# Kernel tuning notes

Measured on AMD Instinct MI355X. Metric: run time of the kernel, lower is better.

## Reference

```python
import jax, jax.numpy as jnp
import numpy as np

N, E, T, D, A = 16384, 65536, 2048, 64, 6


def _w(k, shape, fan_in):
    return jax.random.normal(k, shape, jnp.float32) / np.sqrt(fan_in)


def setup_inputs() -> dict:
    key = jax.random.key(0)
    ks = jax.random.split(key, 20)
    inp = {}
    inp["x"] = jax.random.normal(ks[0], (N, 3), jnp.float32)
    inp["edge_attr"] = jax.random.normal(ks[1], (E, 7), jnp.float32)
    inp["edge_index"] = jax.random.randint(ks[2], (2, E), 0, N)
    inp["nonring"] = jax.random.randint(ks[3], (T, 4), 0, N)
    inp["hx"] = jnp.zeros((1, D), jnp.float32)
    inp["cx"] = jnp.zeros((1, D), jnp.float32)
    inp["W_lin0"] = _w(ks[4], (D, 3), 3); inp["b_lin0"] = jnp.zeros((D,), jnp.float32)
    inp["W_e1"] = _w(ks[5], (128, 7), 7); inp["b_e1"] = jnp.zeros((128,), jnp.float32)
    inp["W_e2"] = _w(ks[6], (D * D, 128), 128); inp["b_e2"] = jnp.zeros((D * D,), jnp.float32)
    inp["conv_root"] = _w(ks[7], (D, D), D); inp["conv_bias"] = jnp.zeros((D,), jnp.float32)
    inp["gru_Wih"] = _w(ks[8], (3 * D, D), D); inp["gru_Whh"] = _w(ks[9], (3 * D, D), D)
    inp["gru_bih"] = jnp.zeros((3 * D,), jnp.float32); inp["gru_bhh"] = jnp.zeros((3 * D,), jnp.float32)
    inp["s2s_Wih"] = _w(ks[10], (4 * D, 2 * D), 2 * D); inp["s2s_Whh"] = _w(ks[11], (4 * D, D), D)
    inp["s2s_bih"] = jnp.zeros((4 * D,), jnp.float32); inp["s2s_bhh"] = jnp.zeros((4 * D,), jnp.float32)
    inp["mem_Wih"] = _w(ks[12], (4 * D, 2 * D), 2 * D); inp["mem_Whh"] = _w(ks[13], (4 * D, D), D)
    inp["mem_bih"] = jnp.zeros((4 * D,), jnp.float32); inp["mem_bhh"] = jnp.zeros((4 * D,), jnp.float32)
    inp["W_lin1"] = _w(ks[14], (D, 5 * D), 5 * D); inp["b_lin1"] = jnp.zeros((D,), jnp.float32)
    inp["W_lin2"] = _w(ks[15], (A, D), D); inp["b_lin2"] = jnp.zeros((A,), jnp.float32)
    inp["W_lin3"] = _w(ks[16], (1, 3 * D), 3 * D); inp["b_lin3"] = jnp.zeros((1,), jnp.float32)
    return inp


def _lstm_cell(xin, h, c, Wih, Whh, bih, bhh):
    g = xin @ Wih.T + bih + h @ Whh.T + bhh
    i, f, gg, o = jnp.split(g, 4, axis=-1)  # torch gate order i,f,g,o
    c = jax.nn.sigmoid(f) * c + jax.nn.sigmoid(i) * jnp.tanh(gg)
    h = jax.nn.sigmoid(o) * jnp.tanh(c)
    return h, c


def _gru_cell(xin, h, Wih, Whh, bih, bhh):
    gi = xin @ Wih.T + bih
    gh = h @ Whh.T + bhh
    ir, iz, inn = jnp.split(gi, 3, axis=-1)  # torch gate order r,z,n
    hr, hz, hn = jnp.split(gh, 3, axis=-1)
    r = jax.nn.sigmoid(ir + hr)
    z = jax.nn.sigmoid(iz + hz)
    n = jnp.tanh(inn + r * hn)
    return (1.0 - z) * n + z * h


def reference(x, edge_attr, edge_index, nonring, hx, cx,
              W_lin0, b_lin0, W_e1, b_e1, W_e2, b_e2, conv_root, conv_bias,
              gru_Wih, gru_Whh, gru_bih, gru_bhh,
              s2s_Wih, s2s_Whh, s2s_bih, s2s_bhh,
              mem_Wih, mem_Whh, mem_bih, mem_bhh,
              W_lin1, b_lin1, W_lin2, b_lin2, W_lin3, b_lin3):
    src, tgt = edge_index[0], edge_index[1]
    out = jax.nn.relu(x @ W_lin0.T + b_lin0)  # [N, D]
    h = out  # GRU hidden (nodes as batch)
    # edge-conditioned dim x dim matrices (NNConv edge MLP)
    ew = jax.nn.relu(edge_attr @ W_e1.T + b_e1)
    ew = (ew @ W_e2.T + b_e2).reshape(E, D, D)  # [E, D, D]
    cnt = jnp.maximum(jax.ops.segment_sum(jnp.ones((E,), out.dtype), tgt, num_segments=N), 1.0)
    for _ in range(3):
        msg = jnp.einsum('ed,edf->ef', out[src], ew)  # per-edge small matmul
        aggr = jax.ops.segment_sum(msg, tgt, num_segments=N) / cnt[:, None]  # scatter-mean
        m = jax.nn.relu(aggr + out @ conv_root + conv_bias)  # NNConv root + bias, then relu
        h = _gru_cell(m, h, gru_Wih, gru_Whh, gru_bih, gru_bhh)
        out = h
    # Set2Set pooling (single graph, B=1), processing_steps=3
    hs = jnp.zeros((1, D), out.dtype)
    cs = jnp.zeros((1, D), out.dtype)
    q_star = jnp.zeros((1, 2 * D), out.dtype)
    for _ in range(3):
        hs, cs = _lstm_cell(q_star, hs, cs, s2s_Wih, s2s_Whh, s2s_bih, s2s_bhh)
        a = jax.nn.softmax(out @ hs[0])  # [N]
        r = (a[:, None] * out).sum(0, keepdims=True)  # [1, D]
        q_star = jnp.concatenate([hs, r], axis=1)
    pool = q_star  # [1, 2D]
    lstm_out, cx_new = _lstm_cell(pool, hx, cx, mem_Wih, mem_Whh, mem_bih, mem_bhh)
    hx_new = lstm_out
    # torsion head: index_select -> view(4*D, -1) -> permute(1,0)
    sel = out[nonring.reshape(-1)]  # [4T, D]
    tfeat = sel.reshape(4 * D, -1).T  # [T, 4D], faithful to torch view semantics
    rep = jnp.repeat(lstm_out.reshape(-1), T).reshape(T, D)  # torch repeat_interleave + view
    pf = jnp.concatenate([tfeat, rep], axis=1)  # [T, 5D]
    logits = jax.nn.relu(pf @ W_lin1.T + b_lin1) @ W_lin2.T + b_lin2  # [T, A]
    v = jnp.concatenate([pool, lstm_out], axis=1) @ W_lin3.T + b_lin3  # [1, 1]
    return logits, v, hx_new, cx_new
```

## Files before the change

### kernel.cpp

```cpp
#include <hip/hip_runtime.h>

#define cN 16384
#define cE 65536
#define cT 2048
#define CAP 88

typedef __attribute__((ext_vector_type(8))) short short8;
typedef __attribute__((ext_vector_type(4))) float f32x4;
typedef __attribute__((ext_vector_type(4))) unsigned u32x4;

__device__ __forceinline__ short f2bf(float f){
  unsigned u = __float_as_uint(f);
  u = (u + 0x7FFFu + ((u >> 16) & 1u)) >> 16;
  return (short)u;
}
__device__ __forceinline__ float bf2f(short s){
  return __uint_as_float(((unsigned)(unsigned short)s) << 16);
}
__device__ __forceinline__ unsigned cvtpk(float lo, float hi){
  unsigned r;
  asm("v_cvt_pk_bf16_f32 %0, %1, %2" : "=v"(r) : "v"(lo), "v"(hi));
  return r;
}
__device__ __forceinline__ float sigm(float x){ return 1.f / (1.f + __expf(-x)); }
__device__ __forceinline__ float wred(float v){
  v += __shfl_xor(v, 32); v += __shfl_xor(v, 16); v += __shfl_xor(v, 8);
  v += __shfl_xor(v, 4);  v += __shfl_xor(v, 2);  v += __shfl_xor(v, 1);
  return v;
}
__device__ __forceinline__ float wredmax(float v){
  v = fmaxf(v, __shfl_xor(v, 32)); v = fmaxf(v, __shfl_xor(v, 16));
  v = fmaxf(v, __shfl_xor(v, 8));  v = fmaxf(v, __shfl_xor(v, 4));
  v = fmaxf(v, __shfl_xor(v, 2));  v = fmaxf(v, __shfl_xor(v, 1));
  return v;
}

#define B_L0   4096
#define B_H1   20480
#define B_W2   22528
#define B_B2   22544
#define B_WP   22656
#define B_DEG  22912
__global__ __launch_bounds__(256) void k_setup(
    const float* __restrict__ x, const float* __restrict__ Wl0, const float* __restrict__ bl0,
    float* __restrict__ out,
    const float* __restrict__ ea, const float* __restrict__ We1, const float* __restrict__ be1,
    unsigned* __restrict__ h1p,
    const float* __restrict__ W2, short* __restrict__ w2f,
    const float* __restrict__ b2, short* __restrict__ b2f,
    const float* __restrict__ convW, const float* __restrict__ gWih,
    const float* __restrict__ gWhh, short* __restrict__ wpk,
    const int* __restrict__ ei, int* __restrict__ deg)
{
  int b = blockIdx.x, tid = threadIdx.x;
  if (b < B_L0){
    int i = b * 256 + tid;
    int n = i >> 6, f = i & 63;
    float acc = bl0[f] + x[n*3]*Wl0[f*3] + x[n*3+1]*Wl0[f*3+1] + x[n*3+2]*Wl0[f*3+2];
    out[i] = fmaxf(acc, 0.f);
  } else if (b < B_H1){
    int i = (b - B_L0) * 256 + tid;
    int e = i >> 6, k = i & 63;
    const float* a  = ea + e * 7;
    const float* w0 = We1 + k * 7;
    const float* w1 = We1 + (k + 64) * 7;
    float a0 = be1[k], a1 = be1[k + 64];
    #pragma unroll
    for (int c = 0; c < 7; c++){ float av = a[c]; a0 += av * w0[c]; a1 += av * w1[c]; }
    unsigned lo = (unsigned short)f2bf(fmaxf(a0, 0.f));
    unsigned hi = (unsigned short)f2bf(fmaxf(a1, 0.f));
    h1p[i] = lo | (hi << 16);
  } else if (b < B_W2){
    int o = (b - B_H1) * 256 + tid;
    int j = o & 7, l = (o >> 3) & 63, ks = (o >> 9) & 31, c = (o >> 14) & 7, fb = (o >> 17) & 3;
    int f = fb * 16 + (l & 15);
    int d = c * 8 + j;
    int k = ks * 4 + ((l >> 4) & 3);
    w2f[o] = f2bf(W2[(d * 64 + f) * 128 + k]);
  } else if (b < B_B2){
    int o = (b - B_W2) * 256 + tid;
    int j = o & 7, l = (o >> 3) & 63, ks2 = (o >> 9) & 1, fb = (o >> 10) & 3;
    int d = ks2 * 32 + ((l >> 4) & 3) * 8 + j;
    int f = fb * 16 + (l & 15);
    b2f[o] = f2bf(b2[d * 64 + f]);
  } else if (b < B_WP){
    int o = (b - B_B2) * 256 + tid;
    int j = o & 7, l = (o >> 3) & 63, kc = (o >> 9) & 1, cb = o >> 10;
    int k = kc * 32 + ((l >> 4) & 3) * 8 + j;
    int c16 = l & 15;
    float v;
    if (cb < 4)       v = convW[k * 64 + cb * 16 + c16];
    else if (cb < 16) v = gWih[((cb - 4) * 16 + c16) * 64 + k];
    else              v = gWhh[((cb - 16) * 16 + c16) * 64 + k];
    wpk[o] = f2bf(v);
  } else {
    int e = (b - B_WP) * 256 + tid;
    atomicAdd(&deg[ei[cE + e]], 1);
  }
}

__global__ __launch_bounds__(1024) void k_scan(const int* __restrict__ deg,
    int* __restrict__ rowp, float* __restrict__ cnt)
{
  __shared__ int part[1024];
  int tid = threadIdx.x;
  int base = tid * 16;
  int loc[16]; int s = 0;
  #pragma unroll
  for (int i = 0; i < 16; i++){ loc[i] = s; s += deg[base + i]; }
  part[tid] = s;
  __syncthreads();
  for (int off = 1; off < 1024; off <<= 1){
    int v = (tid >= off) ? part[tid - off] : 0;
    __syncthreads();
    part[tid] += v;
    __syncthreads();
  }
  int inc = part[tid];
  int eb = inc - s;
  #pragma unroll
  for (int i = 0; i < 16; i++){
    rowp[base + i] = eb + loc[i];
    int dv = deg[base + i];
    cnt[base + i] = (float)(dv > 0 ? dv : 1);
  }
  if (tid == 1023) rowp[16384] = inc;
}

__global__ __launch_bounds__(256) void k_scatter(const int* __restrict__ ei,
    const int* __restrict__ rowp, int* __restrict__ cur,
    int* __restrict__ esrc, int* __restrict__ eidx)
{
  int e = blockIdx.x * 256 + threadIdx.x;
  int t = ei[cE + e];
  int pos = rowp[t] + atomicAdd(&cur[t], 1);
  esrc[pos] = ei[e];
  eidx[pos] = e;
}

__global__ __launch_bounds__(256) void k_sagg(const float* __restrict__ outR,
    float* __restrict__ outW,
    const unsigned* __restrict__ h1p, const short* __restrict__ w2f,
    const short* __restrict__ b2f, const short* __restrict__ wpk,
    const float* __restrict__ convB, const float* __restrict__ bih,
    const float* __restrict__ bhh, const float* __restrict__ cnt,
    const int* __restrict__ rowp, const int* __restrict__ esrc,
    const int* __restrict__ eidx)
{
  __shared__ __align__(16) short S[16][1040];
  __shared__ __align__(16) unsigned h1i[CAP][64];
  __shared__ __align__(16) float outsf[CAP][64];
  __shared__ __align__(16) short osb[16][72];
  int tid = threadIdx.x, w = tid >> 6, lane = tid & 63;
  int t0 = blockIdx.x * 16;

  int ebase = rowp[t0];
  int eend  = rowp[t0 + 16];
  int ecnt  = eend - ebase;
  bool fits = (ecnt <= CAP);
  int scnt  = fits ? ecnt : CAP;
  for (int i = w; i < scnt; i += 4){
    int eid = eidx[ebase + i];
    int src = esrc[ebase + i];
    h1i[i][lane] = h1p[(size_t)eid * 64 + lane];
    outsf[i][lane] = outR[(size_t)src * 64 + lane];
  }
  int toff[4], tcnt[4];
  #pragma unroll
  for (int g = 0; g < 4; g++){
    int t = t0 + w * 4 + g;
    int a = rowp[t], b = rowp[t + 1];
    toff[g] = a - ebase; tcnt[g] = b - a;
  }
  __syncthreads();

  #pragma unroll
  for (int g = 0; g < 4; g++){
    int ti = w * 4 + g;
    float os = 0.f;
    int tf = toff[g], tc = tcnt[g];
    for (int p = 0; p < tc; p++){
      int slot = tf + p;
      if (slot < CAP) os += outsf[slot][lane];
      else            os += outR[(size_t)esrc[ebase + slot] * 64 + lane];
    }
    osb[ti][lane] = (short)cvtpk(os, os);
  }

  f32x4 acc[4] = {{0,0,0,0},{0,0,0,0},{0,0,0,0},{0,0,0,0}};
  int arow = lane & 15, kg = lane >> 4;
  for (int c = 0; c < 8; ++c){
    #pragma unroll
    for (int g = 0; g < 4; ++g){
      int ti = w * 4 + g;
      float a0[8], a1[8];
      #pragma unroll
      for (int d = 0; d < 8; d++){ a0[d] = 0.f; a1[d] = 0.f; }
      int tc = tcnt[g], tf = toff[g];
      if (fits){
        #pragma unroll 2
        for (int p = 0; p < tc; ++p){
          int slot = tf + p;
          unsigned u = h1i[slot][lane];
          float h1a = __uint_as_float(u << 16);
          float h1b = __uint_as_float(u & 0xFFFF0000u);
          f32x4 o0 = *(const f32x4*)&outsf[slot][c * 8];
          f32x4 o1 = *(const f32x4*)&outsf[slot][c * 8 + 4];
          a0[0] = fmaf(o0[0], h1a, a0[0]); a1[0] = fmaf(o0[0], h1b, a1[0]);
          a0[1] = fmaf(o0[1], h1a, a0[1]); a1[1] = fmaf(o0[1], h1b, a1[1]);
          a0[2] = fmaf(o0[2], h1a, a0[2]); a1[2] = fmaf(o0[2], h1b, a1[2]);
          a0[3] = fmaf(o0[3], h1a, a0[3]); a1[3] = fmaf(o0[3], h1b, a1[3]);
          a0[4] = fmaf(o1[0], h1a, a0[4]); a1[4] = fmaf(o1[0], h1b, a1[4]);
          a0[5] = fmaf(o1[1], h1a, a0[5]); a1[5] = fmaf(o1[1], h1b, a1[5]);
          a0[6] = fmaf(o1[2], h1a, a0[6]); a1[6] = fmaf(o1[2], h1b, a1[6]);
          a0[7] = fmaf(o1[3], h1a, a0[7]); a1[7] = fmaf(o1[3], h1b, a1[7]);
        }
      } else {
        for (int p = 0; p < tc; ++p){
          int slot = tf + p;
          if (slot < CAP){
            unsigned u = h1i[slot][lane];
            float h1a = __uint_as_float(u << 16);
            float h1b = __uint_as_float(u & 0xFFFF0000u);
            f32x4 o0 = *(const f32x4*)&outsf[slot][c * 8];
            f32x4 o1 = *(const f32x4*)&outsf[slot][c * 8 + 4];
            #pragma unroll
            for (int d = 0; d < 4; d++){
              a0[d] = fmaf(o0[d], h1a, a0[d]); a1[d] = fmaf(o0[d], h1b, a1[d]);
              a0[4+d] = fmaf(o1[d], h1a, a0[4+d]); a1[4+d] = fmaf(o1[d], h1b, a1[4+d]);
            }
          } else {
            int eid = eidx[ebase + slot];
            int src = esrc[ebase + slot];
            unsigned u = h1p[(size_t)eid * 64 + lane];
            float h1a = __uint_as_float(u << 16);
            float h1b = __uint_as_float(u & 0xFFFF0000u);
            #pragma unroll
            for (int d = 0; d < 8; d++){
              float o = outR[(size_t)src * 64 + c * 8 + d];
              a0[d] = fmaf(o, h1a, a0[d]); a1[d] = fmaf(o, h1b, a1[d]);
            }
          }
        }
      }
      u32x4 p0, p1;
      p0[0] = cvtpk(a0[0], a0[1]); p0[1] = cvtpk(a0[2], a0[3]);
      p0[2] = cvtpk(a0[4], a0[5]); p0[3] = cvtpk(a0[6], a0[7]);
      p1[0] = cvtpk(a1[0], a1[1]); p1[1] = cvtpk(a1[2], a1[3]);
      p1[2] = cvtpk(a1[4], a1[5]); p1[3] = cvtpk(a1[6], a1[7]);
      *(u32x4*)&S[ti][lane * 8]       = p0;
      *(u32x4*)&S[ti][512 + lane * 8] = p1;
    }
    __syncthreads();
    const short* bbase = w2f + ((size_t)(w * 8 + c) * 32) * 512 + lane * 8;
    #pragma unroll
    for (int ks8 = 0; ks8 < 8; ++ks8){
      #pragma unroll
      for (int j = 0; j < 4; ++j){
        int ks = ks8 * 4 + j;
        short8 afr = *(const short8*)&S[arow][ks * 32 + kg * 8];
        short8 bfr = *(const short8*)(bbase + (size_t)ks * 512);
        acc[j] = __builtin_amdgcn_mfma_f32_16x16x32_bf16(afr, bfr, acc[j], 0, 0, 0);
      }
    }
    __syncthreads();
  }
  #pragma unroll
  for (int ks2 = 0; ks2 < 2; ++ks2){
    short8 osf = *(const short8*)&osb[arow][ks2 * 32 + kg * 8];
    short8 bfr = *(const short8*)(b2f + ((size_t)((w * 2 + ks2) * 64 + lane)) * 8);
    acc[ks2] = __builtin_amdgcn_mfma_f32_16x16x32_bf16(osf, bfr, acc[ks2], 0, 0, 0);
  }
  f32x4 accT;
  #pragma unroll
  for (int q = 0; q < 4; q++)
    accT[q] = (acc[0][q] + acc[1][q]) + (acc[2][q] + acc[3][q]);

  int fcol = w * 16 + arow;
  int trow = kg * 4;
  short* tA  = (short*)&h1i[0][0];
  short* mAp = tA + 16 * 72;
  for (int i = tid; i < 512; i += 256){
    int r = i >> 5, c2 = (i & 31) * 2;
    float2 v = *(const float2*)&outR[(size_t)(t0 + r) * 64 + c2];
    *(unsigned*)&tA[r * 72 + c2] = cvtpk(v.x, v.y);
  }
  __syncthreads();
  const short8* WF = (const short8*)wpk;
  short8 aof0 = *(const short8*)&tA[arow * 72 + kg * 8];
  short8 aof1 = *(const short8*)&tA[arow * 72 + 32 + kg * 8];
  f32x4 cz = {0.f, 0.f, 0.f, 0.f};
  f32x4 cva0 = __builtin_amdgcn_mfma_f32_16x16x32_bf16(aof0, WF[(w * 2 + 0) * 64 + lane], cz, 0, 0, 0);
  f32x4 cva1 = __builtin_amdgcn_mfma_f32_16x16x32_bf16(aof1, WF[(w * 2 + 1) * 64 + lane], cz, 0, 0, 0);
  float cb_ = convB[fcol];
  #pragma unroll
  for (int q = 0; q < 4; q++){
    int node = t0 + trow + q;
    float icq = 1.0f / fmaxf(cnt[node], 1.0f);
    float m = fmaxf(accT[q] * icq + cva0[q] + cva1[q] + cb_, 0.f);
    mAp[(trow + q) * 72 + fcol] = f2bf(m);
  }
  __syncthreads();
  short8 amf0 = *(const short8*)&mAp[arow * 72 + kg * 8];
  short8 amf1 = *(const short8*)&mAp[arow * 72 + 32 + kg * 8];
  f32x4 gir = {0,0,0,0}, giz = {0,0,0,0}, gin = {0,0,0,0};
  f32x4 ghr = {0,0,0,0}, ghz = {0,0,0,0}, ghn = {0,0,0,0};
  gir = __builtin_amdgcn_mfma_f32_16x16x32_bf16(amf0, WF[((4  + w) * 2 + 0) * 64 + lane], gir, 0, 0, 0);
  gir = __builtin_amdgcn_mfma_f32_16x16x32_bf16(amf1, WF[((4  + w) * 2 + 1) * 64 + lane], gir, 0, 0, 0);
  giz = __builtin_amdgcn_mfma_f32_16x16x32_bf16(amf0, WF[((8  + w) * 2 + 0) * 64 + lane], giz, 0, 0, 0);
  giz = __builtin_amdgcn_mfma_f32_16x16x32_bf16(amf1, WF[((8  + w) * 2 + 1) * 64 + lane], giz, 0, 0, 0);
  gin = __builtin_amdgcn_mfma_f32_16x16x32_bf16(amf0, WF[((12 + w) * 2 + 0) * 64 + lane], gin, 0, 0, 0);
  gin = __builtin_amdgcn_mfma_f32_16x16x32_bf16(amf1, WF[((12 + w) * 2 + 1) * 64 + lane], gin, 0, 0, 0);
  ghr = __builtin_amdgcn_mfma_f32_16x16x32_bf16(aof0, WF[((16 + w) * 2 + 0) * 64 + lane], ghr, 0, 0, 0);
  ghr = __builtin_amdgcn_mfma_f32_16x16x32_bf16(aof1, WF[((16 + w) * 2 + 1) * 64 + lane], ghr, 0, 0, 0);
  ghz = __builtin_amdgcn_mfma_f32_16x16x32_bf16(aof0, WF[((20 + w) * 2 + 0) * 64 + lane], ghz, 0, 0, 0);
  ghz = __builtin_amdgcn_mfma_f32_16x16x32_bf16(aof1, WF[((20 + w) * 2 + 1) * 64 + lane], ghz, 0, 0, 0);
  ghn = __builtin_amdgcn_mfma_f32_16x16x32_bf16(aof0, WF[((24 + w) * 2 + 0) * 64 + lane], ghn, 0, 0, 0);
  ghn = __builtin_amdgcn_mfma_f32_16x16x32_bf16(aof1, WF[((24 + w) * 2 + 1) * 64 + lane], ghn, 0, 0, 0);
  float bir = bih[fcol], biz = bih[64 + fcol], bin_ = bih[128 + fcol];
  float bhr = bhh[fcol], bhz = bhh[64 + fcol], bhn = bhh[128 + fcol];
  #pragma unroll
  for (int q = 0; q < 4; q++){
    size_t node = (size_t)(t0 + trow + q);
    float rr = sigm(gir[q] + bir + ghr[q] + bhr);
    float zz = sigm(giz[q] + biz + ghz[q] + bhz);
    float nn = tanhf(gin[q] + bin_ + rr * (ghn[q] + bhn));
    float o = outR[node * 64 + fcol];
    outW[node * 64 + fcol] = (1.f - zz) * nn + zz * o;
  }
}

__global__ __launch_bounds__(256) void k_dotsF(const float* __restrict__ out,
    const float* __restrict__ Wih, const float* __restrict__ Whh,
    const float* __restrict__ bih, const float* __restrict__ bhh,
    float* __restrict__ scal,
    const float* __restrict__ rbI, const float* __restrict__ bmI, const float* __restrict__ esI,
    float* __restrict__ rbO, float* __restrict__ bmO, float* __restrict__ esO, int st)
{
  __shared__ float q[128];
  __shared__ float hsL[64];
  __shared__ float gsh[4][64];
  __shared__ float hsh[64];
  __shared__ float smax[4];
  __shared__ float otile[64][64];
  __shared__ float sarr[64];
  __shared__ float ebuf[64];
  __shared__ float rpart[4][64];
  __shared__ float redA[4], redB[4];
  const float* pg = scal + st * 256;
  float* pn = scal + (st + 1) * 256;
  int tid = threadIdx.x, gg = tid >> 6, lane = tid & 63;
  if (st > 0){
    float bm = bmI[tid];
    float m = wredmax(bm);
    if (lane == 0) redA[gg] = m;
    __syncthreads();
    float gmax = fmaxf(fmaxf(redA[0], redA[1]), fmaxf(redA[2], redA[3]));
    float ep = wred(__expf(bm - gmax) * esI[tid]);
    if (lane == 0) redB[gg] = ep;
    float racc = 0.f;
    for (int i = 0; i < 64; i++){
      int b = gg * 64 + i;
      racc += __expf(bmI[b] - gmax) * rbI[b * 64 + lane];
    }
    rpart[gg][lane] = racc;
    __syncthreads();
    if (gg == 0){
      float esum = redB[0] + redB[1] + redB[2] + redB[3];
      float r = rpart[0][lane] + rpart[1][lane] + rpart[2][lane] + rpart[3][lane];
      q[64 + lane] = r / esum;
    }
  } else if (gg == 0) q[64 + lane] = 0.f;
  if (gg == 0){ float hs = pg[lane]; q[lane] = hs; hsL[lane] = hs; }
  __syncthreads();
  float2 fq = *(const float2*)&q[2 * lane];
  float hv0 = hsL[lane];
  #pragma unroll 4
  for (int o = 0; o < 64; o++){
    int row = gg * 64 + o;
    float2 wv = *(const float2*)&Wih[(size_t)row * 128 + 2 * lane];
    float s = wv.x * fq.x + wv.y * fq.y + Whh[(size_t)row * 64 + lane] * hv0;
    s = wred(s);
    if (lane == 0) gsh[gg][o] = s;
  }
  __syncthreads();
  if (gg == 0){
    float gi = gsh[0][lane] + bih[lane]       + bhh[lane];
    float gf = gsh[1][lane] + bih[64 + lane]  + bhh[64 + lane];
    float gv = gsh[2][lane] + bih[128 + lane] + bhh[128 + lane];
    float go = gsh[3][lane] + bih[192 + lane] + bhh[192 + lane];
    float cs = pg[64 + lane];
    float cn = sigm(gf) * cs + sigm(gi) * tanhf(gv);
    float hn = sigm(go) * tanhf(cn);
    hsh[lane] = hn;
    if (blockIdx.x == 0){ pn[lane] = hn; pn[64 + lane] = cn; }
  }
  __syncthreads();
  int nbase = blockIdx.x * 64 + gg * 16;
  float hv = hsh[lane];
  float wmax = -3.4e38f;
  #pragma unroll 4
  for (int i = 0; i < 16; i++){
    float v = out[(size_t)(nbase + i) * 64 + lane];
    otile[gg * 16 + i][lane] = v;
    float p = wred(v * hv);
    if (lane == 0) sarr[gg * 16 + i] = p;
    wmax = fmaxf(wmax, p);
  }
  if (lane == 0) smax[gg] = wmax;
  __syncthreads();
  float bm = fmaxf(fmaxf(smax[0], smax[1]), fmaxf(smax[2], smax[3]));
  if (tid < 64) ebuf[tid] = __expf(sarr[tid] - bm);
  __syncthreads();
  float racc = 0.f;
  #pragma unroll 4
  for (int i = 0; i < 16; i++)
    racc += ebuf[gg * 16 + i] * otile[gg * 16 + i][lane];
  rpart[gg][lane] = racc;
  __syncthreads();
  if (gg == 0){
    float r = rpart[0][lane] + rpart[1][lane] + rpart[2][lane] + rpart[3][lane];
    rbO[blockIdx.x * 64 + lane] = r;
  } else if (gg == 1){
    float es = wred(ebuf[lane]);
    if (lane == 0) esO[blockIdx.x] = es;
  } else if (gg == 2 && lane == 0) bmO[blockIdx.x] = bm;
}

__global__ __launch_bounds__(256) void k_smFin(
    const float* __restrict__ rbI, const float* __restrict__ bmI, const float* __restrict__ esI,
    const float* __restrict__ Wih, const float* __restrict__ Whh,
    const float* __restrict__ bih, const float* __restrict__ bhh,
    const float* __restrict__ hx, const float* __restrict__ cx,
    const float* __restrict__ W3, const float* __restrict__ b3,
    float* __restrict__ scal, float* __restrict__ dout)
{
  __shared__ float redA[4], redB[4];
  __shared__ float rpart[4][64];
  __shared__ float pool[128];
  __shared__ float hxs[64];
  __shared__ float gsh[4][64];
  __shared__ float lob[64];
  int tid = threadIdx.x, wid = tid >> 6, lane = tid & 63;
  float bm = bmI[tid];
  float m = wredmax(bm);
  if (lane == 0) redA[wid] = m;
  __syncthreads();
  float gmax = fmaxf(fmaxf(redA[0], redA[1]), fmaxf(redA[2], redA[3]));
  float ep = wred(__expf(bm - gmax) * esI[tid]);
  if (lane == 0) redB[wid] = ep;
  float racc = 0.f;
  for (int i = 0; i < 64; i++){
    int b = wid * 64 + i;
    racc += __expf(bmI[b] - gmax) * rbI[b * 64 + lane];
  }
  rpart[wid][lane] = racc;
  __syncthreads();
  if (wid == 0){
    float esum = redB[0] + redB[1] + redB[2] + redB[3];
    float r = rpart[0][lane] + rpart[1][lane] + rpart[2][lane] + rpart[3][lane];
    pool[lane] = scal[3 * 256 + lane];
    pool[64 + lane] = r / esum;
    hxs[lane] = hx[lane];
  }
  __syncthreads();
  float2 fq = *(const float2*)&pool[2 * lane];
  float hv = hxs[lane];
  #pragma unroll 4
  for (int o = 0; o < 64; o++){
    int row = wid * 64 + o;
    float2 wv = *(const float2*)&Wih[(size_t)row * 128 + 2 * lane];
    float s = wv.x * fq.x + wv.y * fq.y + Whh[(size_t)row * 64 + lane] * hv;
    s = wred(s);
    if (lane == 0) gsh[wid][o] = s;
  }
  __syncthreads();
  if (wid == 0){
    float gi = gsh[0][lane] + bih[lane]       + bhh[lane];
    float gf = gsh[1][lane] + bih[64 + lane]  + bhh[64 + lane];
    float gv = gsh[2][lane] + bih[128 + lane] + bhh[128 + lane];
    float go = gsh[3][lane] + bih[192 + lane] + bhh[192 + lane];
    float cn = sigm(gf) * cx[lane] + sigm(gi) * tanhf(gv);
    float hn = sigm(go) * tanhf(cn);
    dout[12289 + lane] = hn;
    dout[12353 + lane] = cn;
    scal[1024 + lane] = hn;
    lob[lane] = hn;
  }
  __syncthreads();
  if (wid == 0){
    float a = pool[lane] * W3[lane] + pool[64 + lane] * W3[64 + lane]
            + lob[lane] * W3[128 + lane];
    a = wred(a);
    if (lane == 0) dout[12288] = a + b3[0];
  }
}

__global__ __launch_bounds__(256) void k_head(const float* __restrict__ out,
    const int* __restrict__ nr, const float* __restrict__ scal,
    const float* __restrict__ W1, const float* __restrict__ b1,
    const float* __restrict__ W2, const float* __restrict__ b2,
    float* __restrict__ dout)
{
  __shared__ float pf[4][320];
  __shared__ float hb[4][64];
  int tid = threadIdx.x, wid = tid >> 6, lane = tid & 63;
  int t = blockIdx.x * 4 + wid;
  float lo = scal[1024 + (t >> 5)];
  #pragma unroll
  for (int rep = 0; rep < 4; rep++){
    int j = rep * 64 + lane;
    int idx = nr[j * 32 + (t >> 6)];
    pf[wid][j] = out[idx * 64 + (t & 63)];
  }
  pf[wid][256 + lane] = lo;
  __syncthreads();
  float acc = b1[lane];
  const float* w = W1 + lane * 320;
  #pragma unroll 4
  for (int j = 0; j < 320; j++) acc += pf[wid][j] * w[j];
  hb[wid][lane] = fmaxf(acc, 0.f);
  __syncthreads();
  if (lane < 6){
    float a2 = b2[lane];
    const float* w2 = W2 + lane * 64;
    #pragma unroll 4
    for (int f = 0; f < 64; f++) a2 += hb[wid][f] * w2[f];
    dout[t * 6 + lane] = a2;
  }
}

extern "C" void kernel_launch(void* const* d_in, const int* in_sizes, int n_in,
                              void* d_out, int out_size, void* d_ws, size_t ws_size,
                              hipStream_t stream)
{
  const float* x         = (const float*)d_in[0];
  const float* edge_attr = (const float*)d_in[1];
  const int*   ei        = (const int*)d_in[2];
  const int*   nonring   = (const int*)d_in[3];
  const float* hx        = (const float*)d_in[4];
  const float* cx        = (const float*)d_in[5];
  const float* W_lin0 = (const float*)d_in[6];  const float* b_lin0 = (const float*)d_in[7];
  const float* W_e1   = (const float*)d_in[8];  const float* b_e1   = (const float*)d_in[9];
  const float* W_e2   = (const float*)d_in[10]; const float* b_e2   = (const float*)d_in[11];
  const float* convW  = (const float*)d_in[12]; const float* convB  = (const float*)d_in[13];
  const float* gWih   = (const float*)d_in[14]; const float* gWhh   = (const float*)d_in[15];
  const float* gbih   = (const float*)d_in[16]; const float* gbhh   = (const float*)d_in[17];
  const float* sWih   = (const float*)d_in[18]; const float* sWhh   = (const float*)d_in[19];
  const float* sbih   = (const float*)d_in[20]; const float* sbhh   = (const float*)d_in[21];
  const float* mWih   = (const float*)d_in[22]; const float* mWhh   = (const float*)d_in[23];
  const float* mbih   = (const float*)d_in[24]; const float* mbhh   = (const float*)d_in[25];
  const float* W_lin1 = (const float*)d_in[26]; const float* b_lin1 = (const float*)d_in[27];
  const float* W_lin2 = (const float*)d_in[28]; const float* b_lin2 = (const float*)d_in[29];
  const float* W_lin3 = (const float*)d_in[30]; const float* b_lin3 = (const float*)d_in[31];
  float* dout = (float*)d_out;

  char* w = (char*)d_ws;
  float* outb = (float*)w;  w += (size_t)cN * 64 * 4;
  float* outb2= (float*)w;  w += (size_t)cN * 64 * 4;
  unsigned* h1p = (unsigned*)w;  w += (size_t)cE * 64 * 4;
  short* w2f  = (short*)w;  w += (size_t)64 * 8192 * 2;
  short* b2f  = (short*)w;  w += 4096 * 2;
  short* wpk  = (short*)w;  w += 28672 * 2;
  float* cntb = (float*)w;  w += cN * 4;
  float* rbufA= (float*)w;  w += 256 * 64 * 4;
  float* rbufB= (float*)w;  w += 256 * 64 * 4;
  float* bmA  = (float*)w;  w += 256 * 4;
  float* bmB  = (float*)w;  w += 256 * 4;
  float* esA  = (float*)w;  w += 256 * 4;
  float* esB  = (float*)w;  w += 256 * 4;
  float* scal = (float*)w;  w += 1088 * 4;
  int* deg  = (int*)w;  w += cN * 4;
  int* cur  = (int*)w;  w += cN * 4;
  int* rowp = (int*)w;  w += (cN + 1) * 4 + 60;
  int* esrc = (int*)w;  w += cE * 4;
  int* eidx = (int*)w;  w += cE * 4;

  hipMemsetAsync(deg, 0, cN * 4, stream);
  hipMemsetAsync(cur, 0, cN * 4, stream);
  hipMemsetAsync(scal, 0, 1088 * 4, stream);

  k_setup<<<B_DEG, 256, 0, stream>>>(x, W_lin0, b_lin0, outb,
      edge_attr, W_e1, b_e1, h1p, W_e2, w2f, b_e2, b2f,
      convW, gWih, gWhh, wpk, ei, deg);
  k_scan<<<1, 1024, 0, stream>>>(deg, rowp, cntb);
  k_scatter<<<cE / 256, 256, 0, stream>>>(ei, rowp, cur, esrc, eidx);

  k_sagg<<<cN / 16, 256, 0, stream>>>(outb,  outb2, h1p, w2f, b2f, wpk, convB,
      gbih, gbhh, cntb, rowp, esrc, eidx);
  k_sagg<<<cN / 16, 256, 0, stream>>>(outb2, outb,  h1p, w2f, b2f, wpk, convB,
      gbih, gbhh, cntb, rowp, esrc, eidx);
  k_sagg<<<cN / 16, 256, 0, stream>>>(outb,  outb2, h1p, w2f, b2f, wpk, convB,
      gbih, gbhh, cntb, rowp, esrc, eidx);

  k_dotsF<<<cN / 64, 256, 0, stream>>>(outb2, sWih, sWhh, sbih, sbhh, scal,
      rbufA, bmA, esA, rbufA, bmA, esA, 0);
  k_dotsF<<<cN / 64, 256, 0, stream>>>(outb2, sWih, sWhh, sbih, sbhh, scal,
      rbufA, bmA, esA, rbufB, bmB, esB, 1);
  k_dotsF<<<cN / 64, 256, 0, stream>>>(outb2, sWih, sWhh, sbih, sbhh, scal,
      rbufB, bmB, esB, rbufA, bmA, esA, 2);
  k_smFin<<<1, 256, 0, stream>>>(rbufA, bmA, esA,
      mWih, mWhh, mbih, mbhh, hx, cx, W_lin3, b_lin3, scal, dout);

  k_head<<<cT / 4, 256, 0, stream>>>(outb2, nonring, scal, W_lin1, b_lin1, W_lin2, b_lin2, dout);
}
```

Measured before the change: 483.4 us.

## Register-prefetch edge weight tiles in sagg, drop two memsets and scatter rowp load

The aggregation kernel now holds the next 32 B-fragments of the edge-network weight tile in registers and loads the following chunk while the current MFMAs run, instead of reading each fragment from global memory right before use. The launch bound asks for 2 blocks per CU. The scan kernel now seeds the cursor array with row offsets, which removes one memset and the rowp read in scatter. The set2set kernel treats step 0 state as zero, which removes the scal memset. The 32 short8 registers per thread add register pressure and could cause spills or lower occupancy.

```diff
diff --git a/kernel.cpp b/kernel.cpp
--- a/kernel.cpp
+++ b/kernel.cpp
@@ -100,7 +100,7 @@
 }
 
 __global__ __launch_bounds__(1024) void k_scan(const int* __restrict__ deg,
-    int* __restrict__ rowp, float* __restrict__ cnt)
+    int* __restrict__ rowp, int* __restrict__ cur, float* __restrict__ cnt)
 {
   __shared__ int part[1024];
   int tid = threadIdx.x;
@@ -120,7 +120,9 @@
   int eb = inc - s;
   #pragma unroll
   for (int i = 0; i < 16; i++){
-    rowp[base + i] = eb + loc[i];
+    int rv = eb + loc[i];
+    rowp[base + i] = rv;
+    cur[base + i] = rv;
     int dv = deg[base + i];
     cnt[base + i] = (float)(dv > 0 ? dv : 1);
   }
@@ -128,17 +130,16 @@
 }
 
 __global__ __launch_bounds__(256) void k_scatter(const int* __restrict__ ei,
-    const int* __restrict__ rowp, int* __restrict__ cur,
-    int* __restrict__ esrc, int* __restrict__ eidx)
+    int* __restrict__ cur, int* __restrict__ esrc, int* __restrict__ eidx)
 {
   int e = blockIdx.x * 256 + threadIdx.x;
   int t = ei[cE + e];
-  int pos = rowp[t] + atomicAdd(&cur[t], 1);
+  int pos = atomicAdd(&cur[t], 1);
   esrc[pos] = ei[e];
   eidx[pos] = e;
 }
 
-__global__ __launch_bounds__(256) void k_sagg(const float* __restrict__ outR,
+__global__ __launch_bounds__(256, 2) void k_sagg(const float* __restrict__ outR,
     float* __restrict__ outW,
     const unsigned* __restrict__ h1p, const short* __restrict__ w2f,
     const short* __restrict__ b2f, const short* __restrict__ wpk,
@@ -171,6 +172,13 @@
     int t = t0 + w * 4 + g;
     int a = rowp[t], b = rowp[t + 1];
     toff[g] = a - ebase; tcnt[g] = b - a;
+  }
+  short8 breg[32];
+  {
+    const short* bb0 = w2f + ((size_t)(w * 8) * 32) * 512 + lane * 8;
+    #pragma unroll
+    for (int ks = 0; ks < 32; ++ks)
+      breg[ks] = *(const short8*)(bb0 + (size_t)ks * 512);
   }
   __syncthreads();
 
@@ -252,15 +260,16 @@
       *(u32x4*)&S[ti][512 + lane * 8] = p1;
     }
     __syncthreads();
-    const short* bbase = w2f + ((size_t)(w * 8 + c) * 32) * 512 + lane * 8;
+    const short* bbn = w2f + ((size_t)(w * 8 + c + 1) * 32) * 512 + lane * 8;
+    bool more = (c < 7);
     #pragma unroll
     for (int ks8 = 0; ks8 < 8; ++ks8){
       #pragma unroll
       for (int j = 0; j < 4; ++j){
         int ks = ks8 * 4 + j;
         short8 afr = *(const short8*)&S[arow][ks * 32 + kg * 8];
-        short8 bfr = *(const short8*)(bbase + (size_t)ks * 512);
-        acc[j] = __builtin_amdgcn_mfma_f32_16x16x32_bf16(afr, bfr, acc[j], 0, 0, 0);
+        acc[j] = __builtin_amdgcn_mfma_f32_16x16x32_bf16(afr, breg[ks], acc[j], 0, 0, 0);
+        if (more) breg[ks] = *(const short8*)(bbn + (size_t)ks * 512);
       }
     }
     __syncthreads();
@@ -371,7 +380,10 @@
       q[64 + lane] = r / esum;
     }
   } else if (gg == 0) q[64 + lane] = 0.f;
-  if (gg == 0){ float hs = pg[lane]; q[lane] = hs; hsL[lane] = hs; }
+  if (gg == 0){
+    float hs = (st == 0) ? 0.f : pg[lane];
+    q[lane] = hs; hsL[lane] = hs;
+  }
   __syncthreads();
   float2 fq = *(const float2*)&q[2 * lane];
   float hv0 = hsL[lane];
@@ -389,7 +401,7 @@
     float gf = gsh[1][lane] + bih[64 + lane]  + bhh[64 + lane];
     float gv = gsh[2][lane] + bih[128 + lane] + bhh[128 + lane];
     float go = gsh[3][lane] + bih[192 + lane] + bhh[192 + lane];
-    float cs = pg[64 + lane];
+    float cs = (st == 0) ? 0.f : pg[64 + lane];
     float cn = sigm(gf) * cs + sigm(gi) * tanhf(gv);
     float hn = sigm(go) * tanhf(cn);
     hsh[lane] = hn;
@@ -577,14 +589,12 @@
   int* eidx = (int*)w;  w += cE * 4;
 
   hipMemsetAsync(deg, 0, cN * 4, stream);
-  hipMemsetAsync(cur, 0, cN * 4, stream);
-  hipMemsetAsync(scal, 0, 1088 * 4, stream);
 
   k_setup<<<B_DEG, 256, 0, stream>>>(x, W_lin0, b_lin0, outb,
       edge_attr, W_e1, b_e1, h1p, W_e2, w2f, b_e2, b2f,
       convW, gWih, gWhh, wpk, ei, deg);
-  k_scan<<<1, 1024, 0, stream>>>(deg, rowp, cntb);
-  k_scatter<<<cE / 256, 256, 0, stream>>>(ei, rowp, cur, esrc, eidx);
+  k_scan<<<1, 1024, 0, stream>>>(deg, rowp, cur, cntb);
+  k_scatter<<<cE / 256, 256, 0, stream>>>(ei, cur, esrc, eidx);
 
   k_sagg<<<cN / 16, 256, 0, stream>>>(outb,  outb2, h1p, w2f, b2f, wpk, convB,
       gbih, gbhh, cntb, rowp, esrc, eidx);
```

New measurement: 499.6 us. 1.03x slower.
